# Performance work log

Hardware: AMD Instinct MI355X
Metric: run time of the kernel (lower is better)

Reference implementation:

```python
import jax, jax.numpy as jnp
import numpy as np

N, C_IN, T, V = 64, 64, 256, 25
S = 3            # num_subsets
C_OUT = 128
GROUPS = 8
EPS = 1e-5


def setup_inputs() -> dict:
    key = jax.random.key(0)
    ks = jax.random.split(key, 6)
    x = jax.random.normal(ks[0], (N, C_IN, T, V), dtype=jnp.float32)
    A = jax.random.uniform(ks[1], (S, V, V), dtype=jnp.float32) / V  # normalized-ish adjacency buffer
    PA = jax.random.normal(ks[2], (S, V, V), dtype=jnp.float32) * 0.01  # learnable adjacency offset
    cin_g = C_IN // GROUPS  # 8 input channels per group
    Wg = jax.random.normal(ks[3], (C_OUT * S, cin_g), dtype=jnp.float32) * (1.0 / np.sqrt(cin_g))
    bg = jax.random.normal(ks[4], (C_OUT * S,), dtype=jnp.float32) * 0.01
    gamma = jnp.ones((C_OUT,), dtype=jnp.float32)
    beta = jnp.zeros((C_OUT,), dtype=jnp.float32)
    return {"x": x, "A": A, "PA": PA, "Wg": Wg, "bg": bg, "gamma": gamma, "beta": beta}


def reference(x, A, PA, Wg, bg, gamma, beta):
    n, c, t, v = x.shape
    cin_g = c // GROUPS
    cout_total = Wg.shape[0]          # C_OUT * S
    cout_g = cout_total // GROUPS
    # grouped 1x1 conv: conv_group
    xg = x.reshape(n, GROUPS, cin_g, t, v)
    Wg_ = Wg.reshape(GROUPS, cout_g, cin_g)
    out = jnp.einsum('ngctv,gdc->ngdtv', xg, Wg_).reshape(n, cout_total, t, v)
    out = out + bg[None, :, None, None]
    # split into subsets and apply per-subset adjacency, accumulate
    outs = out.reshape(n, S, cout_total // S, t, v)   # (N,S,Cout,T,V)
    Aeff = A + PA                                      # (S,V,V)
    total = jnp.einsum('nsctv,svw->nctw', outs, Aeff)  # (N,Cout,T,V)
    # BatchNorm2d (training-mode batch statistics, biased variance)
    mean = total.mean(axis=(0, 2, 3), keepdims=True)
    var = ((total - mean) ** 2).mean(axis=(0, 2, 3), keepdims=True)
    y = (total - mean) * jax.lax.rsqrt(var + EPS)
    return y * gamma[None, :, None, None] + beta[None, :, None, None]
```

## Files before the change

### kernel.cpp

```cpp
#include <hip/hip_runtime.h>
#include <math.h>

#define NB   64
#define CIN  64
#define TDIM 256
#define VV   25
#define SS   3
#define COUT 128
#define NTV  (NB * TDIM * VV)
#define OUT_TOTAL (NB * COUT * TDIM * VV)
#define TT   8
#define NTILE (TDIM / TT)

#define WS_STATS 0
#define WS_AE2   2048
#define WS_W2    4160
#define WS_BIAS  7232
#define WS_SCALE 10816
#define WS_SHIFT 10944
#define MID_OFF  16384

__device__ __forceinline__ void fma4(float4& a, float s, const float4& b) {
    a.x = fmaf(s, b.x, a.x);
    a.y = fmaf(s, b.y, a.y);
    a.z = fmaf(s, b.z, a.z);
    a.w = fmaf(s, b.w, a.w);
}

__global__ void prep_kernel(const float* __restrict__ A, const float* __restrict__ PA,
                            const float* __restrict__ Wg, const float* __restrict__ bg,
                            float* __restrict__ ws) {
    const int tid = threadIdx.x;
    for (int i = tid; i < 2048; i += 256) ws[WS_STATS + i] = 0.0f;
    for (int i = tid; i < 25 * 84; i += 256) {
        int v = i / 84, r = i % 84;
        int s = r / 28, w = r % 28;
        float val = 0.0f;
        if (w < 25) {
            int idx = s * 625 + v * 25 + w;
            val = A[idx] + PA[idx];
        }
        ws[WS_AE2 + i] = val;
    }
    for (int i = tid; i < 24 * 128; i += 256) {
        int row = i / 128, c = i % 128;
        int s = row / 8, j = row % 8;
        ws[WS_W2 + i] = Wg[(s * 128 + c) * 8 + j];
    }
    for (int i = tid; i < 128 * 28; i += 256) {
        int c = i / 28, w = i % 28;
        float val = 0.0f;
        if (w < 25) {
            for (int s = 0; s < 3; ++s) {
                float cs = 0.0f;
                for (int v = 0; v < 25; ++v) {
                    int idx = s * 625 + v * 25 + w;
                    cs += A[idx] + PA[idx];
                }
                val += bg[s * 128 + c] * cs;
            }
        }
        ws[WS_BIAS + i] = val;
    }
}

template <bool PERM>
__global__ __launch_bounds__(256, 3)
void main_kernel(const float* __restrict__ x, float* __restrict__ ws,
                 float* __restrict__ out, float* __restrict__ mid) {
    __shared__ __align__(16) float s_x[25 * 68];
    __shared__ __align__(16) float s_ae[25 * 84];
    __shared__ __align__(16) float s_w[24 * 128];
    __shared__ __align__(16) float s_y[3 * 64 * 28];
    __shared__ float s_stats[256];

    const int tid = threadIdx.x;
    const int bid = blockIdx.x;
    const int xcd   = bid & 7;
    const int j     = bid >> 3;
    const int ttile = xcd * 4 + (j & 3);
    const int n     = j >> 2;
    const int t0    = ttile * TT;

    s_stats[tid] = 0.0f;
    for (int i = tid; i < 25 * 84; i += 256) s_ae[i] = ws[WS_AE2 + i];
    for (int i = tid; i < 24 * 128; i += 256) s_w[i] = ws[WS_W2 + i];

    const bool active = tid < 224;
    int c0 = 0, w0 = 0;
    float4 b0 = {0,0,0,0}, b1 = b0, b2 = b0, b3 = b0;
    if (active) {
        int ct = tid & 31, wt = tid >> 5;
        c0 = ct * 4;
        w0 = wt * 4;
        b0 = *(const float4*)&ws[WS_BIAS + (c0 + 0) * 28 + w0];
        b1 = *(const float4*)&ws[WS_BIAS + (c0 + 1) * 28 + w0];
        b2 = *(const float4*)&ws[WS_BIAS + (c0 + 2) * 28 + w0];
        b3 = *(const float4*)&ws[WS_BIAS + (c0 + 3) * 28 + w0];
    }
    float st1[4] = {0, 0, 0, 0};
    float st2[4] = {0, 0, 0, 0};

    const float* xbase = x + (size_t)n * (CIN * TDIM * VV);
    float* obase = out + (size_t)n * (COUT * TDIM * VV);
    float* mbase = mid + ((size_t)n * NTILE + ttile) * (TT * COUT * VV);

    for (int tt = 0; tt < TT; ++tt) {
        const int t = t0 + tt;
        const float* xb = xbase + t * VV;
        for (int i = tid; i < 64 * 25; i += 256) {
            int cin = i / 25, v = i % 25;
            s_x[v * 68 + cin] = xb[cin * (TDIM * VV) + v];
        }
        __syncthreads();

        for (int task = tid; task < 336; task += 256) {
            int cint = task & 15, swt = task >> 4;
            int cin0 = cint * 4, sw0 = swt * 4;
            float4 a0 = {0, 0, 0, 0}, a1 = a0, a2 = a0, a3 = a0;
            #pragma unroll
            for (int v = 0; v < 25; ++v) {
                float4 xv = *(const float4*)&s_x[v * 68 + cin0];
                float4 av = *(const float4*)&s_ae[v * 84 + sw0];
                fma4(a0, xv.x, av);
                fma4(a1, xv.y, av);
                fma4(a2, xv.z, av);
                fma4(a3, xv.w, av);
            }
            int s = sw0 / 28, w = sw0 % 28;
            int yb = (s * 64 + cin0) * 28 + w;
            *(float4*)&s_y[yb]      = a0;
            *(float4*)&s_y[yb + 28] = a1;
            *(float4*)&s_y[yb + 56] = a2;
            *(float4*)&s_y[yb + 84] = a3;
        }
        __syncthreads();

        float4 r0, r1, r2, r3;
        if (active) {
            r0 = b0; r1 = b1; r2 = b2; r3 = b3;
            #pragma unroll
            for (int s = 0; s < 3; ++s) {
                int g = (s * 128 + c0) / 48;
                int yb = (s * 64 + g * 8) * 28 + w0;
                int wb = s * 8 * 128 + c0;
                #pragma unroll
                for (int jj = 0; jj < 8; ++jj) {
                    float4 wv = *(const float4*)&s_w[wb + jj * 128];
                    float4 yv = *(const float4*)&s_y[yb + jj * 28];
                    fma4(r0, wv.x, yv);
                    fma4(r1, wv.y, yv);
                    fma4(r2, wv.z, yv);
                    fma4(r3, wv.w, yv);
                }
            }
            float4 rr[4] = {r0, r1, r2, r3};
            #pragma unroll
            for (int a = 0; a < 4; ++a) {
                float4 v = rr[a];
                if (w0 + 3 < 25) {
                    st1[a] += v.x + v.y + v.z + v.w;
                    st2[a] += v.x * v.x + v.y * v.y + v.z * v.z + v.w * v.w;
                } else {
                    st1[a] += v.x;
                    st2[a] += v.x * v.x;
                }
            }
        }
        __syncthreads();

        if (active) {
            float4 rr[4] = {r0, r1, r2, r3};
            #pragma unroll
            for (int a = 0; a < 4; ++a) {
                int base = (c0 + a) * 25 + w0;
                s_y[base] = rr[a].x;
                if (w0 + 3 < 25) {
                    s_y[base + 1] = rr[a].y;
                    s_y[base + 2] = rr[a].z;
                    s_y[base + 3] = rr[a].w;
                }
            }
        }
        __syncthreads();

        if (PERM) {
            float4* mb = (float4*)(mbase + tt * (COUT * VV));
            const float4* sy = (const float4*)s_y;
            for (int i = tid; i < 128 * 25 / 4; i += 256) mb[i] = sy[i];
        } else {
            float* ob = obase + t * VV;
            for (int i = tid; i < 128 * 25; i += 256) {
                int c = i / 25, w = i % 25;
                ob[c * (TDIM * VV) + w] = s_y[i];
            }
        }
    }

    if (active) {
        #pragma unroll
        for (int a = 0; a < 4; ++a) {
            atomicAdd(&s_stats[c0 + a], st1[a]);
            atomicAdd(&s_stats[128 + c0 + a], st2[a]);
        }
    }
    __syncthreads();
    if (tid < 128) {
        float* st = ws + WS_STATS + xcd * 256;
        atomicAdd(&st[tid], s_stats[tid]);
        atomicAdd(&st[128 + tid], s_stats[128 + tid]);
    }
}

__global__ void finalize_kernel(const float* __restrict__ gamma,
                                const float* __restrict__ beta,
                                float* __restrict__ ws) {
    const int c = threadIdx.x;
    if (c < 128) {
        float s = 0.0f, q = 0.0f;
        for (int k = 0; k < 8; ++k) {
            s += ws[WS_STATS + k * 256 + c];
            q += ws[WS_STATS + k * 256 + 128 + c];
        }
        const float inv = 1.0f / (float)NTV;
        float mean = s * inv;
        float var = q * inv - mean * mean;
        float sc = gamma[c] * rsqrtf(var + 1e-5f);
        ws[WS_SCALE + c] = sc;
        ws[WS_SHIFT + c] = beta[c] - mean * sc;
    }
}

__global__ __launch_bounds__(256)
void norm_perm(const float* __restrict__ mid, float* __restrict__ out,
               const float* __restrict__ ws) {
    const int bid = blockIdx.x;
    const int n = bid >> 7;
    const int c = bid & 127;
    const float sc = ws[WS_SCALE + c];
    const float sh = ws[WS_SHIFT + c];
    float* ob = out + ((size_t)n * COUT + c) * (TDIM * VV);
    const float* mb = mid + (size_t)n * (TDIM * COUT * VV) + c * VV;
    const int tid = threadIdx.x;
    #pragma unroll
    for (int k = 0; k < 25; ++k) {
        int i = k * 256 + tid;
        int t = i / 25, v = i - t * 25;
        float val = mb[(size_t)t * (COUT * VV) + v];
        ob[i] = fmaf(val, sc, sh);
    }
}

__global__ __launch_bounds__(256)
void norm_inplace(float* __restrict__ out, const float* __restrict__ ws) {
    const int total4 = OUT_TOTAL / 4;
    const int stride = gridDim.x * blockDim.x;
    for (int i = blockIdx.x * blockDim.x + threadIdx.x; i < total4; i += stride) {
        int c = (i / 1600) & 127;
        float sc = ws[WS_SCALE + c];
        float sh = ws[WS_SHIFT + c];
        float4 v = ((float4*)out)[i];
        v.x = fmaf(v.x, sc, sh);
        v.y = fmaf(v.y, sc, sh);
        v.z = fmaf(v.z, sc, sh);
        v.w = fmaf(v.w, sc, sh);
        ((float4*)out)[i] = v;
    }
}

extern "C" void kernel_launch(void* const* d_in, const int* in_sizes, int n_in,
                              void* d_out, int out_size, void* d_ws, size_t ws_size,
                              hipStream_t stream) {
    const float* x     = (const float*)d_in[0];
    const float* A     = (const float*)d_in[1];
    const float* PA    = (const float*)d_in[2];
    const float* Wg    = (const float*)d_in[3];
    const float* bg    = (const float*)d_in[4];
    const float* gamma = (const float*)d_in[5];
    const float* beta  = (const float*)d_in[6];
    float* out = (float*)d_out;
    float* ws  = (float*)d_ws;
    float* mid = ws + MID_OFF;

    const bool perm = ws_size >= ((size_t)MID_OFF + (size_t)OUT_TOTAL) * sizeof(float);

    prep_kernel<<<1, 256, 0, stream>>>(A, PA, Wg, bg, ws);
    if (perm) {
        main_kernel<true><<<NB * NTILE, 256, 0, stream>>>(x, ws, out, mid);
        finalize_kernel<<<1, 128, 0, stream>>>(gamma, beta, ws);
        norm_perm<<<NB * COUT, 256, 0, stream>>>(mid, out, ws);
    } else {
        main_kernel<false><<<NB * NTILE, 256, 0, stream>>>(x, ws, out, mid);
        finalize_kernel<<<1, 128, 0, stream>>>(gamma, beta, ws);
        norm_inplace<<<4096, 256, 0, stream>>>(out, ws);
    }
}
```

Baseline: 1.250 ms.

## Prefetch next x slice into registers, write results directly, restage norm via LDS

The main kernel now loads the next time step's x slice into registers while the current step computes, then stores it to shared memory after the first barrier. This removes one barrier and the serialized load per step. Results go straight from registers to global memory, using a [w][c] layout in the mid buffer, instead of a shared-memory staging pass and two extra barriers. norm_perm now handles 4 channels per block: it reads float4 groups across channels into shared memory and writes coalesced float4 outputs, with the grid shrunk to match. The cost is more registers and fewer, larger norm blocks.

```diff
diff --git a/kernel.cpp b/kernel.cpp
--- a/kernel.cpp
+++ b/kernel.cpp
@@ -105,14 +105,41 @@
     float* obase = out + (size_t)n * (COUT * TDIM * VV);
     float* mbase = mid + ((size_t)n * NTILE + ttile) * (TT * COUT * VV);
 
+    int offg[7], offl[7];
+    #pragma unroll
+    for (int m = 0; m < 6; ++m) {
+        int i = tid + 256 * m;
+        int cin = i / 25, v = i - cin * 25;
+        offg[m] = cin * (TDIM * VV) + v;
+        offl[m] = v * 68 + cin;
+    }
+    {
+        int i = tid + 1536;
+        int cin = i / 25, v = i - cin * 25;
+        offg[6] = (tid < 64) ? cin * (TDIM * VV) + v : 0;
+        offl[6] = v * 68 + cin;
+    }
+    const bool has7 = (tid < 64);
+
+    float xr[7];
+    {
+        const float* xb = xbase + (size_t)t0 * VV;
+        #pragma unroll
+        for (int m = 0; m < 6; ++m) xr[m] = xb[offg[m]];
+        if (has7) xr[6] = xb[offg[6]];
+        #pragma unroll
+        for (int m = 0; m < 6; ++m) s_x[offl[m]] = xr[m];
+        if (has7) s_x[offl[6]] = xr[6];
+    }
+    __syncthreads();
+
     for (int tt = 0; tt < TT; ++tt) {
-        const int t = t0 + tt;
-        const float* xb = xbase + t * VV;
-        for (int i = tid; i < 64 * 25; i += 256) {
-            int cin = i / 25, v = i % 25;
-            s_x[v * 68 + cin] = xb[cin * (TDIM * VV) + v];
-        }
-        __syncthreads();
+        if (tt < TT - 1) {
+            const float* xb = xbase + (size_t)(t0 + tt + 1) * VV;
+            #pragma unroll
+            for (int m = 0; m < 6; ++m) xr[m] = xb[offg[m]];
+            if (has7) xr[6] = xb[offg[6]];
+        }
 
         for (int task = tid; task < 336; task += 256) {
             int cint = task & 15, swt = task >> 4;
@@ -136,9 +163,14 @@
         }
         __syncthreads();
 
-        float4 r0, r1, r2, r3;
+        if (tt < TT - 1) {
+            #pragma unroll
+            for (int m = 0; m < 6; ++m) s_x[offl[m]] = xr[m];
+            if (has7) s_x[offl[6]] = xr[6];
+        }
+
         if (active) {
-            r0 = b0; r1 = b1; r2 = b2; r3 = b3;
+            float4 r0 = b0, r1 = b1, r2 = b2, r3 = b3;
             #pragma unroll
             for (int s = 0; s < 3; ++s) {
                 int g = (s * 128 + c0) / 48;
@@ -158,7 +190,7 @@
             #pragma unroll
             for (int a = 0; a < 4; ++a) {
                 float4 v = rr[a];
-                if (w0 + 3 < 25) {
+                if (w0 < 24) {
                     st1[a] += v.x + v.y + v.z + v.w;
                     st2[a] += v.x * v.x + v.y * v.y + v.z * v.z + v.w * v.w;
                 } else {
@@ -166,35 +198,34 @@
                     st2[a] += v.x * v.x;
                 }
             }
+            if (PERM) {
+                float* mt = mbase + tt * (COUT * VV);
+                *(float4*)&mt[(w0 + 0) * COUT + c0] =
+                    make_float4(r0.x, r1.x, r2.x, r3.x);
+                if (w0 < 24) {
+                    *(float4*)&mt[(w0 + 1) * COUT + c0] =
+                        make_float4(r0.y, r1.y, r2.y, r3.y);
+                    *(float4*)&mt[(w0 + 2) * COUT + c0] =
+                        make_float4(r0.z, r1.z, r2.z, r3.z);
+                    *(float4*)&mt[(w0 + 3) * COUT + c0] =
+                        make_float4(r0.w, r1.w, r2.w, r3.w);
+                }
+            } else {
+                float* ob = obase + (size_t)(t0 + tt) * VV;
+                #pragma unroll
+                for (int a = 0; a < 4; ++a) {
+                    float4 v = rr[a];
+                    float* row = ob + (size_t)(c0 + a) * (TDIM * VV);
+                    row[w0] = v.x;
+                    if (w0 < 24) {
+                        row[w0 + 1] = v.y;
+                        row[w0 + 2] = v.z;
+                        row[w0 + 3] = v.w;
+                    }
+                }
+            }
         }
         __syncthreads();
-
-        if (active) {
-            float4 rr[4] = {r0, r1, r2, r3};
-            #pragma unroll
-            for (int a = 0; a < 4; ++a) {
-                int base = (c0 + a) * 25 + w0;
-                s_y[base] = rr[a].x;
-                if (w0 + 3 < 25) {
-                    s_y[base + 1] = rr[a].y;
-                    s_y[base + 2] = rr[a].z;
-                    s_y[base + 3] = rr[a].w;
-                }
-            }
-        }
-        __syncthreads();
-
-        if (PERM) {
-            float4* mb = (float4*)(mbase + tt * (COUT * VV));
-            const float4* sy = (const float4*)s_y;
-            for (int i = tid; i < 128 * 25 / 4; i += 256) mb[i] = sy[i];
-        } else {
-            float* ob = obase + t * VV;
-            for (int i = tid; i < 128 * 25; i += 256) {
-                int c = i / 25, w = i % 25;
-                ob[c * (TDIM * VV) + w] = s_y[i];
-            }
-        }
     }
 
     if (active) {
@@ -234,20 +265,57 @@
 __global__ __launch_bounds__(256)
 void norm_perm(const float* __restrict__ mid, float* __restrict__ out,
                const float* __restrict__ ws) {
+    __shared__ __align__(16) float sb[4 * 1600];
+    const int tid = threadIdx.x;
     const int bid = blockIdx.x;
-    const int n = bid >> 7;
-    const int c = bid & 127;
-    const float sc = ws[WS_SCALE + c];
-    const float sh = ws[WS_SHIFT + c];
-    float* ob = out + ((size_t)n * COUT + c) * (TDIM * VV);
-    const float* mb = mid + (size_t)n * (TDIM * COUT * VV) + c * VV;
-    const int tid = threadIdx.x;
+    const int xcd = bid & 7;
+    const int j   = bid >> 3;
+    const int cq  = xcd * 4 + (j & 3);
+    const int n   = j >> 2;
+    const int c0  = cq * 4;
+
+    float sca[4], sha[4];
     #pragma unroll
-    for (int k = 0; k < 25; ++k) {
-        int i = k * 256 + tid;
-        int t = i / 25, v = i - t * 25;
-        float val = mb[(size_t)t * (COUT * VV) + v];
-        ob[i] = fmaf(val, sc, sh);
+    for (int cl = 0; cl < 4; ++cl) {
+        sca[cl] = ws[WS_SCALE + c0 + cl];
+        sha[cl] = ws[WS_SHIFT + c0 + cl];
+    }
+
+    const float* mb = mid + (size_t)n * (TDIM * COUT * VV) + c0;
+    for (int tc = 0; tc < 4; ++tc) {
+        const float* mc = mb + (size_t)tc * 64 * (COUT * VV);
+        #pragma unroll
+        for (int k = 0; k < 7; ++k) {
+            int idx = k * 256 + tid;
+            if (idx < 1600) {
+                int t = idx / 25;
+                int w = idx - t * 25;
+                float4 v = *(const float4*)&mc[(size_t)t * (COUT * VV) + w * COUT];
+                sb[idx]        = v.x;
+                sb[1600 + idx] = v.y;
+                sb[3200 + idx] = v.z;
+                sb[4800 + idx] = v.w;
+            }
+        }
+        __syncthreads();
+        #pragma unroll
+        for (int cl = 0; cl < 4; ++cl) {
+            float4* ob = (float4*)out + (size_t)(n * COUT + c0 + cl) * 1600 + tc * 400;
+            const float4* sv = (const float4*)&sb[cl * 1600];
+            #pragma unroll
+            for (int k = 0; k < 2; ++k) {
+                int idx = k * 256 + tid;
+                if (idx < 400) {
+                    float4 v = sv[idx];
+                    v.x = fmaf(v.x, sca[cl], sha[cl]);
+                    v.y = fmaf(v.y, sca[cl], sha[cl]);
+                    v.z = fmaf(v.z, sca[cl], sha[cl]);
+                    v.w = fmaf(v.w, sca[cl], sha[cl]);
+                    ob[idx] = v;
+                }
+            }
+        }
+        __syncthreads();
     }
 }
 
@@ -288,7 +356,7 @@
     if (perm) {
         main_kernel<true><<<NB * NTILE, 256, 0, stream>>>(x, ws, out, mid);
         finalize_kernel<<<1, 128, 0, stream>>>(gamma, beta, ws);
-        norm_perm<<<NB * COUT, 256, 0, stream>>>(mid, out, ws);
+        norm_perm<<<NB * 32, 256, 0, stream>>>(mid, out, ws);
     } else {
         main_kernel<false><<<NB * NTILE, 256, 0, stream>>>(x, ws, out, mid);
         finalize_kernel<<<1, 128, 0, stream>>>(gamma, beta, ws);
```

Result: slower. 2.212 ms (+77.0%).

## Software-pipeline x loads across time steps and drop per-step barriers

Applied to the files above, without the earlier changes.

Restructures the per-timestep loop so the next timestep's x slice is prefetched into registers while the current step's channel mixing runs. Results go to a new dedicated shared buffer, which removes the write-after-read hazard on s_y and cuts the number of __syncthreads per step from four to two. The adjacency stage for the next step is computed after the store, and launch bounds are relaxed from 3 to 2 blocks per SM to make room for the extra registers and shared memory. The cost is more LDS use and possibly lower occupancy.

```diff
diff --git a/kernel.cpp b/kernel.cpp
--- a/kernel.cpp
+++ b/kernel.cpp
@@ -65,13 +65,14 @@
 }
 
 template <bool PERM>
-__global__ __launch_bounds__(256, 3)
+__global__ __launch_bounds__(256, 2)
 void main_kernel(const float* __restrict__ x, float* __restrict__ ws,
                  float* __restrict__ out, float* __restrict__ mid) {
     __shared__ __align__(16) float s_x[25 * 68];
     __shared__ __align__(16) float s_ae[25 * 84];
     __shared__ __align__(16) float s_w[24 * 128];
     __shared__ __align__(16) float s_y[3 * 64 * 28];
+    __shared__ __align__(16) float s_res[128 * 25];
     __shared__ float s_stats[256];
 
     const int tid = threadIdx.x;
@@ -105,40 +106,53 @@
     float* obase = out + (size_t)n * (COUT * TDIM * VV);
     float* mbase = mid + ((size_t)n * NTILE + ttile) * (TT * COUT * VV);
 
-    for (int tt = 0; tt < TT; ++tt) {
-        const int t = t0 + tt;
-        const float* xb = xbase + t * VV;
+    {
+        const float* xb = xbase + (size_t)t0 * VV;
         for (int i = tid; i < 64 * 25; i += 256) {
             int cin = i / 25, v = i % 25;
             s_x[v * 68 + cin] = xb[cin * (TDIM * VV) + v];
         }
-        __syncthreads();
-
-        for (int task = tid; task < 336; task += 256) {
-            int cint = task & 15, swt = task >> 4;
-            int cin0 = cint * 4, sw0 = swt * 4;
-            float4 a0 = {0, 0, 0, 0}, a1 = a0, a2 = a0, a3 = a0;
-            #pragma unroll
-            for (int v = 0; v < 25; ++v) {
-                float4 xv = *(const float4*)&s_x[v * 68 + cin0];
-                float4 av = *(const float4*)&s_ae[v * 84 + sw0];
-                fma4(a0, xv.x, av);
-                fma4(a1, xv.y, av);
-                fma4(a2, xv.z, av);
-                fma4(a3, xv.w, av);
-            }
-            int s = sw0 / 28, w = sw0 % 28;
-            int yb = (s * 64 + cin0) * 28 + w;
-            *(float4*)&s_y[yb]      = a0;
-            *(float4*)&s_y[yb + 28] = a1;
-            *(float4*)&s_y[yb + 56] = a2;
-            *(float4*)&s_y[yb + 84] = a3;
-        }
-        __syncthreads();
-
-        float4 r0, r1, r2, r3;
+    }
+    __syncthreads();
+
+    for (int task = tid; task < 336; task += 256) {
+        int cint = task & 15, swt = task >> 4;
+        int cin0 = cint * 4, sw0 = swt * 4;
+        float4 a0 = {0, 0, 0, 0}, a1 = a0, a2 = a0, a3 = a0;
+        #pragma unroll
+        for (int v = 0; v < 25; ++v) {
+            float4 xv = *(const float4*)&s_x[v * 68 + cin0];
+            float4 av = *(const float4*)&s_ae[v * 84 + sw0];
+            fma4(a0, xv.x, av);
+            fma4(a1, xv.y, av);
+            fma4(a2, xv.z, av);
+            fma4(a3, xv.w, av);
+        }
+        int s = sw0 / 28, w = sw0 % 28;
+        int yb = (s * 64 + cin0) * 28 + w;
+        *(float4*)&s_y[yb]      = a0;
+        *(float4*)&s_y[yb + 28] = a1;
+        *(float4*)&s_y[yb + 56] = a2;
+        *(float4*)&s_y[yb + 84] = a3;
+    }
+    __syncthreads();
+
+    for (int tt = 0; tt < TT; ++tt) {
+        float xr[7];
+        if (tt < TT - 1) {
+            const float* xb = xbase + (size_t)(t0 + tt + 1) * VV;
+            #pragma unroll
+            for (int m = 0; m < 7; ++m) {
+                int i = tid + 256 * m;
+                if (i < 1600) {
+                    int cin = i / 25, v = i - cin * 25;
+                    xr[m] = xb[cin * (TDIM * VV) + v];
+                }
+            }
+        }
+
         if (active) {
-            r0 = b0; r1 = b1; r2 = b2; r3 = b3;
+            float4 r0 = b0, r1 = b1, r2 = b2, r3 = b3;
             #pragma unroll
             for (int s = 0; s < 3; ++s) {
                 int g = (s * 128 + c0) / 48;
@@ -166,19 +180,25 @@
                     st2[a] += v.x * v.x;
                 }
             }
-        }
-        __syncthreads();
-
-        if (active) {
-            float4 rr[4] = {r0, r1, r2, r3};
             #pragma unroll
             for (int a = 0; a < 4; ++a) {
                 int base = (c0 + a) * 25 + w0;
-                s_y[base] = rr[a].x;
+                s_res[base] = rr[a].x;
                 if (w0 + 3 < 25) {
-                    s_y[base + 1] = rr[a].y;
-                    s_y[base + 2] = rr[a].z;
-                    s_y[base + 3] = rr[a].w;
+                    s_res[base + 1] = rr[a].y;
+                    s_res[base + 2] = rr[a].z;
+                    s_res[base + 3] = rr[a].w;
+                }
+            }
+        }
+
+        if (tt < TT - 1) {
+            #pragma unroll
+            for (int m = 0; m < 7; ++m) {
+                int i = tid + 256 * m;
+                if (i < 1600) {
+                    int cin = i / 25, v = i - cin * 25;
+                    s_x[v * 68 + cin] = xr[m];
                 }
             }
         }
@@ -186,15 +206,39 @@
 
         if (PERM) {
             float4* mb = (float4*)(mbase + tt * (COUT * VV));
-            const float4* sy = (const float4*)s_y;
-            for (int i = tid; i < 128 * 25 / 4; i += 256) mb[i] = sy[i];
+            const float4* sr = (const float4*)s_res;
+            for (int i = tid; i < 128 * 25 / 4; i += 256) mb[i] = sr[i];
         } else {
-            float* ob = obase + t * VV;
+            float* ob = obase + (size_t)(t0 + tt) * VV;
             for (int i = tid; i < 128 * 25; i += 256) {
                 int c = i / 25, w = i % 25;
-                ob[c * (TDIM * VV) + w] = s_y[i];
-            }
-        }
+                ob[c * (TDIM * VV) + w] = s_res[i];
+            }
+        }
+
+        if (tt < TT - 1) {
+            for (int task = tid; task < 336; task += 256) {
+                int cint = task & 15, swt = task >> 4;
+                int cin0 = cint * 4, sw0 = swt * 4;
+                float4 a0 = {0, 0, 0, 0}, a1 = a0, a2 = a0, a3 = a0;
+                #pragma unroll
+                for (int v = 0; v < 25; ++v) {
+                    float4 xv = *(const float4*)&s_x[v * 68 + cin0];
+                    float4 av = *(const float4*)&s_ae[v * 84 + sw0];
+                    fma4(a0, xv.x, av);
+                    fma4(a1, xv.y, av);
+                    fma4(a2, xv.z, av);
+                    fma4(a3, xv.w, av);
+                }
+                int s = sw0 / 28, w = sw0 % 28;
+                int yb = (s * 64 + cin0) * 28 + w;
+                *(float4*)&s_y[yb]      = a0;
+                *(float4*)&s_y[yb + 28] = a1;
+                *(float4*)&s_y[yb + 56] = a2;
+                *(float4*)&s_y[yb + 84] = a3;
+            }
+        }
+        __syncthreads();
     }
 
     if (active) {
```

New measurement: 1.091 ms. 12.7% less time.
